# Kernel optimization log

Measured on AMD Instinct MI355X. Metric: run time of the kernel, lower is better.

## Reference

```python
import jax, jax.numpy as jnp
import numpy as np

N_NODES = 50000
N_REL = 8
IN_DIM = 128
HID = 128
N_EDGES = 800000
N_TRIP = 100000


def setup_inputs() -> dict:
    key = jax.random.key(0)
    ks = jax.random.split(key, 12)
    s = 0.05
    return {
        "emb": jax.random.normal(ks[0], (N_NODES, IN_DIM), jnp.float32),
        "W0": jax.random.normal(ks[1], (N_REL, IN_DIM, HID), jnp.float32) * s,
        "root0": jax.random.normal(ks[2], (IN_DIM, HID), jnp.float32) * s,
        "b0": jnp.zeros((HID,), jnp.float32),
        "W1": jax.random.normal(ks[3], (N_REL, HID, HID), jnp.float32) * s,
        "root1": jax.random.normal(ks[4], (HID, HID), jnp.float32) * s,
        "b1": jnp.zeros((HID,), jnp.float32),
        "rel_emb": jax.random.normal(ks[5], (N_REL, HID), jnp.float32),
        "edge_index": jax.random.randint(ks[6], (2, N_EDGES), 0, N_NODES, jnp.int64 if jax.config.read('jax_enable_x64') else jnp.int32),
        "edge_type": jax.random.randint(ks[7], (N_EDGES,), 0, N_REL, jnp.int32),
        "head_idx": jax.random.randint(ks[8], (N_TRIP,), 0, N_NODES, jnp.int32),
        "rel_idx": jax.random.randint(ks[9], (N_TRIP,), 0, N_REL, jnp.int32),
        "tail_idx": jax.random.randint(ks[10], (N_TRIP,), 0, N_NODES, jnp.int32),
    }


def _rgcn_layer(h, W, root, bias, src, dst, edge_type):
    # PyG RGCNConv: per-relation MEAN aggregation of neighbor features at dst,
    # transformed by the relation weight, plus root transform and bias.
    # Mean commutes with the linear map, so aggregate raw features first.
    n, r = N_NODES, N_REL
    seg = dst * r + edge_type  # (E,) joint (dst, relation) segment id
    msg = h[src]               # (E, d) irregular gather
    sums = jax.ops.segment_sum(msg, seg, num_segments=n * r)          # (N*R, d)
    cnt = jax.ops.segment_sum(jnp.ones((src.shape[0],), h.dtype), seg,
                              num_segments=n * r)                     # (N*R,)
    mean = (sums / jnp.maximum(cnt, 1.0)[:, None]).reshape(n, r, -1)  # (N, R, d)
    return jnp.einsum('nrd,rdh->nh', mean, W) + h @ root + bias


def reference(emb, W0, root0, b0, W1, root1, b1, rel_emb,
              edge_index, edge_type, head_idx, rel_idx, tail_idx):
    src = edge_index[0]
    dst = edge_index[1]
    et = edge_type.astype(jnp.int32)
    h = emb
    h = jax.nn.relu(_rgcn_layer(h, W0, root0, b0, src, dst, et))
    h = jax.nn.relu(_rgcn_layer(h, W1, root1, b1, src, dst, et))
    # DistMult score: sum(h_head * r * h_tail)
    score = jnp.sum(h[head_idx] * rel_emb[rel_idx] * h[tail_idx], axis=-1)
    return score
```

## Files before the change

### kernel.cpp

```cpp
#include <hip/hip_runtime.h>
#include <hip/hip_bf16.h>

#define N_NODES 50000
#define N_REL   8
#define DIM     128
#define N_EDGES 800000
#define N_TRIP  100000
#define NSEG    (N_NODES * N_REL)
#define NBUCKET 196
#define CAP     6144

typedef __attribute__((ext_vector_type(8))) short bf16x8;
typedef __attribute__((ext_vector_type(4))) float f32x4;

static __device__ __forceinline__ unsigned short f2b(float f) {
    __hip_bfloat16 h = __float2bfloat16(f);
    return *reinterpret_cast<unsigned short*>(&h);
}
static __device__ __forceinline__ float blo(unsigned int u) {
    return __uint_as_float(u << 16);
}
static __device__ __forceinline__ float bhi(unsigned int u) {
    return __uint_as_float(u & 0xffff0000u);
}
static __device__ __forceinline__ int lds_off(int row, int chunk) {
    return (row * 16 + (chunk ^ (row & 7))) * 8;
}

__global__ __launch_bounds__(256) void bucket_scatter(
        const int* __restrict__ edge_index,
        const int* __restrict__ edge_type,
        int* __restrict__ gcnt,
        unsigned int* __restrict__ slack) {
    __shared__ int hist[NBUCKET];
    __shared__ int cur[NBUCKET];
    int tid = threadIdx.x;
    for (int i = tid; i < NBUCKET; i += 256) hist[i] = 0;
    __syncthreads();
    int base = blockIdx.x * 4096;
    unsigned int w[16];
    int bk[16];
    #pragma unroll
    for (int i = 0; i < 16; ++i) {
        int e = base + i * 256 + tid;
        if (e < N_EDGES) {
            int src = edge_index[e];
            int dst = edge_index[N_EDGES + e];
            int r = edge_type[e];
            w[i] = (unsigned int)src | ((unsigned int)r << 16) |
                   ((unsigned int)(dst & 255) << 19);
            bk[i] = dst >> 8;
            atomicAdd(&hist[bk[i]], 1);
        } else {
            bk[i] = -1;
        }
    }
    __syncthreads();
    for (int i = tid; i < NBUCKET; i += 256)
        cur[i] = atomicAdd(&gcnt[i], hist[i]);
    __syncthreads();
    #pragma unroll
    for (int i = 0; i < 16; ++i) {
        if (bk[i] >= 0) {
            int p = atomicAdd(&cur[bk[i]], 1);
            if (p < CAP) slack[(size_t)bk[i] * CAP + p] = w[i];
        }
    }
}

__global__ void bucket_scan(const int* __restrict__ gcnt,
                            int* __restrict__ gbase,
                            int* __restrict__ offsets) {
    __shared__ int sh[256];
    int t = threadIdx.x;
    int v = (t < NBUCKET) ? gcnt[t] : 0;
    sh[t] = v;
    __syncthreads();
    #pragma unroll
    for (int off = 1; off < 256; off <<= 1) {
        int x = (t >= off) ? sh[t - off] : 0;
        __syncthreads();
        sh[t] += x;
        __syncthreads();
    }
    if (t < NBUCKET) gbase[t] = sh[t] - v;
    if (t == 0) offsets[NSEG] = N_EDGES;
}

__global__ __launch_bounds__(256) void bucket_sort(
        const unsigned int* __restrict__ slack,
        const int* __restrict__ gcnt,
        const int* __restrict__ gbase,
        unsigned int* __restrict__ sorted_pack,
        int* __restrict__ offsets,
        float* __restrict__ invcnt) {
    __shared__ unsigned int ebuf[CAP];
    __shared__ unsigned int obuf[CAP];
    __shared__ int hist[2048];
    __shared__ int excl[2048];
    __shared__ int sh[256];
    int b = blockIdx.x, t = threadIdx.x;
    int n = gcnt[b]; if (n > CAP) n = CAP;
    int bb = gbase[b];
    for (int i = t; i < n; i += 256) ebuf[i] = slack[(size_t)b * CAP + i];
    for (int i = t; i < 2048; i += 256) hist[i] = 0;
    __syncthreads();
    for (int i = t; i < n; i += 256) {
        unsigned int w = ebuf[i];
        int seg = (int)((w >> 19) << 3) | (int)((w >> 16) & 7u);
        atomicAdd(&hist[seg], 1);
    }
    __syncthreads();
    int c[8];
    int s = 0;
    #pragma unroll
    for (int j = 0; j < 8; ++j) { c[j] = hist[t * 8 + j]; s += c[j]; }
    sh[t] = s;
    __syncthreads();
    #pragma unroll
    for (int off = 1; off < 256; off <<= 1) {
        int x = (t >= off) ? sh[t - off] : 0;
        __syncthreads();
        sh[t] += x;
        __syncthreads();
    }
    int ex = sh[t] - s;
    #pragma unroll
    for (int j = 0; j < 8; ++j) { excl[t * 8 + j] = ex; ex += c[j]; }
    __syncthreads();
    #pragma unroll
    for (int j = 0; j < 8; ++j) hist[t * 8 + j] = excl[t * 8 + j];
    __syncthreads();
    for (int i = t; i < n; i += 256) {
        unsigned int w = ebuf[i];
        int seg = (int)((w >> 19) << 3) | (int)((w >> 16) & 7u);
        int p = atomicAdd(&hist[seg], 1);
        obuf[p] = w & 0x7ffffu;
    }
    __syncthreads();
    for (int i = t; i < n; i += 256) sorted_pack[bb + i] = obuf[i];
    int segbase = b * 2048;
    #pragma unroll
    for (int j = 0; j < 8; ++j) {
        int gseg = segbase + t * 8 + j;
        if (gseg < NSEG) {
            offsets[gseg] = bb + excl[t * 8 + j];
            invcnt[gseg] = (c[j] > 0) ? 1.0f / (float)c[j] : 0.f;
        }
    }
}

__global__ void cvt_emb_kernel(const float* __restrict__ src,
                               unsigned short* __restrict__ dst) {
    int i = blockIdx.x * blockDim.x + threadIdx.x;
    const int npair = N_NODES * DIM / 2;
    if (i >= npair) return;
    float2 v = ((const float2*)src)[i];
    unsigned int p = (unsigned int)f2b(v.x) | ((unsigned int)f2b(v.y) << 16);
    ((unsigned int*)dst)[i] = p;
}

__global__ void cvt_w2_kernel(const float* __restrict__ root0,
                              const float* __restrict__ W0,
                              const float* __restrict__ root1,
                              const float* __restrict__ W1,
                              unsigned short* __restrict__ Wt2a,
                              unsigned short* __restrict__ Wt2b) {
    int s = blockIdx.x;
    int n = blockIdx.y;
    int k = threadIdx.x;
    const float* root = blockIdx.z ? root1 : root0;
    const float* W    = blockIdx.z ? W1 : W0;
    unsigned short* Wt2 = blockIdx.z ? Wt2b : Wt2a;
    float v = (s == 0) ? root[k * 128 + n]
                       : W[((size_t)(s - 1) * 128 + k) * 128 + n];
    Wt2[((size_t)s * 128 + n) * 128 + k] = f2b(v);
}

__global__ __launch_bounds__(256) void gemm9_bn32(
        const unsigned short* __restrict__ hb,
        const unsigned short* __restrict__ Wt2,
        unsigned short* __restrict__ Y) {
    __shared__ unsigned short Bs[32 * 16 * 8];

    int tid = threadIdx.x;
    int wave = tid >> 6, lane = tid & 63;
    int wm = wave & 1, wn = wave >> 1;
    int quad = lane >> 4, l16 = lane & 15;
    int row0 = blockIdx.x * 64;
    int col0 = blockIdx.y * 32;

    bf16x8 afr[2][4];
    #pragma unroll
    for (int i = 0; i < 2; ++i) {
        int grow = row0 + wm * 32 + i * 16 + l16;
        if (grow >= N_NODES) grow = N_NODES - 1;
        #pragma unroll
        for (int kk = 0; kk < 4; ++kk)
            afr[i][kk] = *(const bf16x8*)(hb + (size_t)grow * DIM + kk * 32 + quad * 8);
    }

    for (int s = 0; s < 9; ++s) {
        __syncthreads();
        {
            int n = tid >> 3, c0 = (tid & 7) * 2;
            const unsigned short* gp = Wt2 + ((size_t)s * 128 + col0 + n) * 128 + c0 * 8;
            #pragma unroll
            for (int q = 0; q < 2; ++q)
                *(bf16x8*)&Bs[lds_off(n, c0 + q)] = *(const bf16x8*)(gp + q * 8);
        }
        __syncthreads();

        f32x4 acc[2];
        #pragma unroll
        for (int i = 0; i < 2; ++i) acc[i] = (f32x4){0.f, 0.f, 0.f, 0.f};

        #pragma unroll
        for (int kk = 0; kk < 4; ++kk) {
            int chunk = kk * 4 + quad;
            bf16x8 bfr = *(const bf16x8*)&Bs[lds_off(wn * 16 + l16, chunk)];
            #pragma unroll
            for (int i = 0; i < 2; ++i)
                acc[i] = __builtin_amdgcn_mfma_f32_16x16x32_bf16(
                    afr[i][kk], bfr, acc[i], 0, 0, 0);
        }

        unsigned short* Ys = Y + (size_t)s * N_NODES * 128;
        #pragma unroll
        for (int i = 0; i < 2; ++i) {
            int gr0 = row0 + wm * 32 + i * 16 + quad * 4;
            int gc = col0 + wn * 16 + l16;
            #pragma unroll
            for (int r = 0; r < 4; ++r) {
                int grow = gr0 + r;
                if (grow < N_NODES)
                    Ys[(size_t)grow * 128 + gc] = f2b(acc[i][r]);
            }
        }
    }
}

__global__ __launch_bounds__(256) void aggregate_out(
        const unsigned short* __restrict__ Y,
        const float* __restrict__ bias,
        const int* __restrict__ offsets,
        const unsigned int* __restrict__ sorted_pack,
        const float* __restrict__ invcnt,
        unsigned short* __restrict__ hout) {
    int dst = blockIdx.x * 4 + (threadIdx.x >> 6);
    if (dst >= N_NODES) return;
    int lane = threadIdx.x & 63;
    const unsigned int* Yu = (const unsigned int*)Y;

    unsigned int r0 = Yu[(size_t)dst * 64 + lane];
    float a0 = blo(r0), a1 = bhi(r0);

    int beg = offsets[dst * N_REL];
    int end = offsets[dst * N_REL + N_REL];
    for (int base = beg; base < end; base += 64) {
        int np = end - base; if (np > 64) np = 64;
        unsigned int pk = 0; float ivl = 0.f;
        if (lane < np) {
            pk = sorted_pack[base + lane];
            ivl = invcnt[dst * N_REL + (int)(pk >> 16)];
        }
        int j = 0;
        for (; j + 7 < np; j += 8) {
            unsigned int pp[8]; float ii[8];
            #pragma unroll
            for (int q = 0; q < 8; ++q) {
                pp[q] = __shfl((int)pk, j + q, 64);
                ii[q] = __shfl(ivl, j + q, 64);
            }
            unsigned int vv[8];
            #pragma unroll
            for (int q = 0; q < 8; ++q)
                vv[q] = Yu[((size_t)(1 + (pp[q] >> 16)) * N_NODES + (pp[q] & 0xffffu)) * 64 + lane];
            #pragma unroll
            for (int q = 0; q < 8; ++q) {
                a0 = fmaf(blo(vv[q]), ii[q], a0);
                a1 = fmaf(bhi(vv[q]), ii[q], a1);
            }
        }
        for (; j < np; ++j) {
            unsigned int pj = __shfl((int)pk, j, 64);
            float ij = __shfl(ivl, j, 64);
            unsigned int v = Yu[((size_t)(1 + (pj >> 16)) * N_NODES + (pj & 0xffffu)) * 64 + lane];
            a0 = fmaf(blo(v), ij, a0); a1 = fmaf(bhi(v), ij, a1);
        }
    }
    float2 bv = ((const float2*)bias)[lane];
    a0 = fmaxf(a0 + bv.x, 0.f);
    a1 = fmaxf(a1 + bv.y, 0.f);
    unsigned int po = (unsigned int)f2b(a0) | ((unsigned int)f2b(a1) << 16);
    ((unsigned int*)(hout + (size_t)dst * DIM))[lane] = po;
}

__global__ void score_kernel(const unsigned short* __restrict__ hb,
                             const float* __restrict__ rel_emb,
                             const int* __restrict__ head,
                             const int* __restrict__ rel,
                             const int* __restrict__ tail,
                             float* __restrict__ out) {
    int t = blockIdx.x * 4 + (threadIdx.x >> 6);
    if (t >= N_TRIP) return;
    int lane = threadIdx.x & 63;
    unsigned int ph = ((const unsigned int*)(hb + (size_t)head[t] * DIM))[lane];
    unsigned int pt = ((const unsigned int*)(hb + (size_t)tail[t] * DIM))[lane];
    float2 rr = ((const float2*)(rel_emb + (size_t)rel[t] * DIM))[lane];
    float s = blo(ph) * rr.x * blo(pt) + bhi(ph) * rr.y * bhi(pt);
    #pragma unroll
    for (int off = 32; off; off >>= 1) s += __shfl_xor(s, off, 64);
    if (lane == 0) out[t] = s;
}

extern "C" void kernel_launch(void* const* d_in, const int* in_sizes, int n_in,
                              void* d_out, int out_size, void* d_ws, size_t ws_size,
                              hipStream_t stream) {
    const float* emb     = (const float*)d_in[0];
    const float* W0      = (const float*)d_in[1];
    const float* root0   = (const float*)d_in[2];
    const float* b0      = (const float*)d_in[3];
    const float* W1      = (const float*)d_in[4];
    const float* root1   = (const float*)d_in[5];
    const float* b1      = (const float*)d_in[6];
    const float* rel_emb = (const float*)d_in[7];
    const int* edge_index = (const int*)d_in[8];
    const int* edge_type  = (const int*)d_in[9];
    const int* head_idx   = (const int*)d_in[10];
    const int* rel_idx    = (const int*)d_in[11];
    const int* tail_idx   = (const int*)d_in[12];
    float* out = (float*)d_out;

    char* p = (char*)d_ws;
    size_t y_bytes   = (size_t)9 * N_NODES * DIM * sizeof(unsigned short);
    size_t hb_bytes  = (size_t)N_NODES * DIM * sizeof(unsigned short);
    size_t wt2_bytes = (size_t)9 * 128 * 128 * sizeof(unsigned short);
    unsigned short* Y    = (unsigned short*)p; p += y_bytes;
    unsigned short* embb = (unsigned short*)p; p += hb_bytes;
    unsigned short* h1b  = (unsigned short*)p; p += hb_bytes;
    unsigned short* h2b  = (unsigned short*)p; p += hb_bytes;
    unsigned short* Wt2a = (unsigned short*)p; p += wt2_bytes;
    unsigned short* Wt2b = (unsigned short*)p; p += wt2_bytes;
    int* offsets = (int*)p;           p += (size_t)(NSEG + 1) * sizeof(int);
    float* invcnt = (float*)p;        p += (size_t)NSEG * sizeof(float);
    unsigned int* sorted_pack = (unsigned int*)p; p += (size_t)N_EDGES * sizeof(unsigned int);
    unsigned int* slack = (unsigned int*)p; p += (size_t)NBUCKET * CAP * sizeof(unsigned int);
    int* gcnt  = (int*)p;             p += (size_t)NBUCKET * sizeof(int);
    int* gbase = (int*)p;
    (void)ws_size; (void)in_sizes; (void)n_in; (void)out_size;

    dim3 blk256(256);

    hipMemsetAsync(gcnt, 0, (size_t)NBUCKET * sizeof(int), stream);
    bucket_scatter<<<(N_EDGES + 4095) / 4096, blk256, 0, stream>>>(edge_index, edge_type,
                                                                   gcnt, slack);
    bucket_scan<<<1, 256, 0, stream>>>(gcnt, gbase, offsets);
    bucket_sort<<<NBUCKET, blk256, 0, stream>>>(slack, gcnt, gbase, sorted_pack,
                                                offsets, invcnt);

    cvt_emb_kernel<<<(N_NODES * DIM / 2 + 255) / 256, blk256, 0, stream>>>(emb, embb);
    cvt_w2_kernel<<<dim3(9, 128, 2), 128, 0, stream>>>(root0, W0, root1, W1, Wt2a, Wt2b);

    dim3 ggrid((N_NODES + 63) / 64, 4);
    int agrid = (N_NODES + 3) / 4;

    gemm9_bn32<<<ggrid, blk256, 0, stream>>>(embb, Wt2a, Y);
    aggregate_out<<<agrid, blk256, 0, stream>>>(Y, b0, offsets, sorted_pack, invcnt, h1b);

    gemm9_bn32<<<ggrid, blk256, 0, stream>>>(h1b, Wt2b, Y);
    aggregate_out<<<agrid, blk256, 0, stream>>>(Y, b1, offsets, sorted_pack, invcnt, h2b);

    score_kernel<<<(N_TRIP + 3) / 4, blk256, 0, stream>>>(h2b, rel_emb, head_idx, rel_idx,
                                                          tail_idx, out);
}
```

Before: 314.3 us.

## Fuse per-relation mean aggregation with MFMA transform, dropping the 9-slice intermediate

```diff
diff --git a/kernel.cpp b/kernel.cpp
--- a/kernel.cpp
+++ b/kernel.cpp
@@ -6,9 +6,10 @@
 #define DIM     128
 #define N_EDGES 800000
 #define N_TRIP  100000
-#define NSEG    (N_NODES * N_REL)
-#define NBUCKET 196
-#define CAP     6144
+#define NDBLK   196
+#define NB2     (N_REL * NDBLK)
+#define CAP2    1024
+#define NOFF    (N_REL * N_NODES + 1)
 
 typedef __attribute__((ext_vector_type(8))) short bf16x8;
 typedef __attribute__((ext_vector_type(4))) float f32x4;
@@ -32,10 +33,10 @@
         const int* __restrict__ edge_type,
         int* __restrict__ gcnt,
         unsigned int* __restrict__ slack) {
-    __shared__ int hist[NBUCKET];
-    __shared__ int cur[NBUCKET];
+    __shared__ int hist[NB2];
+    __shared__ int cur[NB2];
     int tid = threadIdx.x;
-    for (int i = tid; i < NBUCKET; i += 256) hist[i] = 0;
+    for (int i = tid; i < NB2; i += 256) hist[i] = 0;
     __syncthreads();
     int base = blockIdx.x * 4096;
     unsigned int w[16];
@@ -47,34 +48,40 @@
             int src = edge_index[e];
             int dst = edge_index[N_EDGES + e];
             int r = edge_type[e];
-            w[i] = (unsigned int)src | ((unsigned int)r << 16) |
-                   ((unsigned int)(dst & 255) << 19);
-            bk[i] = dst >> 8;
+            w[i] = (unsigned int)src | ((unsigned int)(dst & 255) << 16);
+            bk[i] = r * NDBLK + (dst >> 8);
             atomicAdd(&hist[bk[i]], 1);
         } else {
             bk[i] = -1;
         }
     }
     __syncthreads();
-    for (int i = tid; i < NBUCKET; i += 256)
+    for (int i = tid; i < NB2; i += 256)
         cur[i] = atomicAdd(&gcnt[i], hist[i]);
     __syncthreads();
     #pragma unroll
     for (int i = 0; i < 16; ++i) {
         if (bk[i] >= 0) {
             int p = atomicAdd(&cur[bk[i]], 1);
-            if (p < CAP) slack[(size_t)bk[i] * CAP + p] = w[i];
+            if (p < CAP2) slack[(size_t)bk[i] * CAP2 + p] = w[i];
         }
     }
 }
 
 __global__ void bucket_scan(const int* __restrict__ gcnt,
                             int* __restrict__ gbase,
-                            int* __restrict__ offsets) {
+                            int* __restrict__ offR) {
     __shared__ int sh[256];
     int t = threadIdx.x;
-    int v = (t < NBUCKET) ? gcnt[t] : 0;
-    sh[t] = v;
+    int c[8];
+    int s = 0;
+    #pragma unroll
+    for (int j = 0; j < 8; ++j) {
+        int idx = t * 8 + j;
+        int v = (idx < NB2) ? gcnt[idx] : 0;
+        c[j] = v; s += v;
+    }
+    sh[t] = s;
     __syncthreads();
     #pragma unroll
     for (int off = 1; off < 256; off <<= 1) {
@@ -83,71 +90,60 @@
         sh[t] += x;
         __syncthreads();
     }
-    if (t < NBUCKET) gbase[t] = sh[t] - v;
-    if (t == 0) offsets[NSEG] = N_EDGES;
+    int ex = sh[t] - s;
+    #pragma unroll
+    for (int j = 0; j < 8; ++j) {
+        int idx = t * 8 + j;
+        if (idx < NB2) gbase[idx] = ex;
+        ex += c[j];
+    }
+    if (t == 0) offR[N_REL * N_NODES] = N_EDGES;
 }
 
 __global__ __launch_bounds__(256) void bucket_sort(
         const unsigned int* __restrict__ slack,
         const int* __restrict__ gcnt,
         const int* __restrict__ gbase,
-        unsigned int* __restrict__ sorted_pack,
-        int* __restrict__ offsets,
-        float* __restrict__ invcnt) {
-    __shared__ unsigned int ebuf[CAP];
-    __shared__ unsigned int obuf[CAP];
-    __shared__ int hist[2048];
-    __shared__ int excl[2048];
+        unsigned int* __restrict__ spack,
+        int* __restrict__ offR) {
+    __shared__ unsigned int ebuf[CAP2];
+    __shared__ unsigned int obuf[CAP2];
+    __shared__ int hist[256];
+    __shared__ int excl[256];
     __shared__ int sh[256];
     int b = blockIdx.x, t = threadIdx.x;
-    int n = gcnt[b]; if (n > CAP) n = CAP;
+    int r = b / NDBLK, dblk = b % NDBLK;
+    int n = gcnt[b]; if (n > CAP2) n = CAP2;
     int bb = gbase[b];
-    for (int i = t; i < n; i += 256) ebuf[i] = slack[(size_t)b * CAP + i];
-    for (int i = t; i < 2048; i += 256) hist[i] = 0;
+    for (int i = t; i < n; i += 256) ebuf[i] = slack[(size_t)b * CAP2 + i];
+    hist[t] = 0;
+    __syncthreads();
+    for (int i = t; i < n; i += 256)
+        atomicAdd(&hist[(ebuf[i] >> 16) & 255], 1);
+    __syncthreads();
+    int c = hist[t];
+    sh[t] = c;
+    __syncthreads();
+    #pragma unroll
+    for (int off = 1; off < 256; off <<= 1) {
+        int x = (t >= off) ? sh[t - off] : 0;
+        __syncthreads();
+        sh[t] += x;
+        __syncthreads();
+    }
+    int ex = sh[t] - c;
+    excl[t] = ex;
+    hist[t] = ex;
     __syncthreads();
     for (int i = t; i < n; i += 256) {
         unsigned int w = ebuf[i];
-        int seg = (int)((w >> 19) << 3) | (int)((w >> 16) & 7u);
-        atomicAdd(&hist[seg], 1);
-    }
-    __syncthreads();
-    int c[8];
-    int s = 0;
-    #pragma unroll
-    for (int j = 0; j < 8; ++j) { c[j] = hist[t * 8 + j]; s += c[j]; }
-    sh[t] = s;
-    __syncthreads();
-    #pragma unroll
-    for (int off = 1; off < 256; off <<= 1) {
-        int x = (t >= off) ? sh[t - off] : 0;
-        __syncthreads();
-        sh[t] += x;
-        __syncthreads();
-    }
-    int ex = sh[t] - s;
-    #pragma unroll
-    for (int j = 0; j < 8; ++j) { excl[t * 8 + j] = ex; ex += c[j]; }
-    __syncthreads();
-    #pragma unroll
-    for (int j = 0; j < 8; ++j) hist[t * 8 + j] = excl[t * 8 + j];
-    __syncthreads();
-    for (int i = t; i < n; i += 256) {
-        unsigned int w = ebuf[i];
-        int seg = (int)((w >> 19) << 3) | (int)((w >> 16) & 7u);
-        int p = atomicAdd(&hist[seg], 1);
-        obuf[p] = w & 0x7ffffu;
-    }
-    __syncthreads();
-    for (int i = t; i < n; i += 256) sorted_pack[bb + i] = obuf[i];
-    int segbase = b * 2048;
-    #pragma unroll
-    for (int j = 0; j < 8; ++j) {
-        int gseg = segbase + t * 8 + j;
-        if (gseg < NSEG) {
-            offsets[gseg] = bb + excl[t * 8 + j];
-            invcnt[gseg] = (c[j] > 0) ? 1.0f / (float)c[j] : 0.f;
-        }
-    }
+        int p = atomicAdd(&hist[(w >> 16) & 255], 1);
+        obuf[p] = w;
+    }
+    __syncthreads();
+    for (int i = t; i < n; i += 256) spack[bb + i] = obuf[i];
+    int dst = dblk * 256 + t;
+    if (dst < N_NODES) offR[r * N_NODES + dst] = bb + excl[t];
 }
 
 __global__ void cvt_emb_kernel(const float* __restrict__ src,
@@ -177,123 +173,144 @@
     Wt2[((size_t)s * 128 + n) * 128 + k] = f2b(v);
 }
 
-__global__ __launch_bounds__(256) void gemm9_bn32(
+__global__ __launch_bounds__(256) void rgcn_fused(
         const unsigned short* __restrict__ hb,
         const unsigned short* __restrict__ Wt2,
-        unsigned short* __restrict__ Y) {
-    __shared__ unsigned short Bs[32 * 16 * 8];
+        const float* __restrict__ bias,
+        const int* __restrict__ offR,
+        const unsigned int* __restrict__ spack,
+        unsigned short* __restrict__ hout) {
+    __shared__ unsigned short Mbuf[64 * 16 * 8];
+    unsigned int* Mb32 = (unsigned int*)Mbuf;
+    const unsigned int* hb32 = (const unsigned int*)hb;
 
     int tid = threadIdx.x;
-    int wave = tid >> 6, lane = tid & 63;
-    int wm = wave & 1, wn = wave >> 1;
+    int wid = tid >> 6, lane = tid & 63;
     int quad = lane >> 4, l16 = lane & 15;
-    int row0 = blockIdx.x * 64;
-    int col0 = blockIdx.y * 32;
-
-    bf16x8 afr[2][4];
-    #pragma unroll
-    for (int i = 0; i < 2; ++i) {
-        int grow = row0 + wm * 32 + i * 16 + l16;
-        if (grow >= N_NODES) grow = N_NODES - 1;
+    int t0 = blockIdx.x * 64;
+    int col0w = wid * 32;
+
+    f32x4 acc[4][2];
+    #pragma unroll
+    for (int mi = 0; mi < 4; ++mi)
+        #pragma unroll
+        for (int ni = 0; ni < 2; ++ni)
+            acc[mi][ni] = (f32x4){0.f, 0.f, 0.f, 0.f};
+
+    {
+        const unsigned short* Wp = Wt2 + ((size_t)(col0w + l16)) * DIM + quad * 8;
+        bf16x8 bf[2][4];
+        #pragma unroll
+        for (int ni = 0; ni < 2; ++ni)
+            #pragma unroll
+            for (int kk = 0; kk < 4; ++kk)
+                bf[ni][kk] = *(const bf16x8*)(Wp + (ni * 16) * DIM + kk * 32);
         #pragma unroll
         for (int kk = 0; kk < 4; ++kk)
-            afr[i][kk] = *(const bf16x8*)(hb + (size_t)grow * DIM + kk * 32 + quad * 8);
-    }
-
-    for (int s = 0; s < 9; ++s) {
-        __syncthreads();
-        {
-            int n = tid >> 3, c0 = (tid & 7) * 2;
-            const unsigned short* gp = Wt2 + ((size_t)s * 128 + col0 + n) * 128 + c0 * 8;
-            #pragma unroll
-            for (int q = 0; q < 2; ++q)
-                *(bf16x8*)&Bs[lds_off(n, c0 + q)] = *(const bf16x8*)(gp + q * 8);
-        }
-        __syncthreads();
-
-        f32x4 acc[2];
-        #pragma unroll
-        for (int i = 0; i < 2; ++i) acc[i] = (f32x4){0.f, 0.f, 0.f, 0.f};
-
-        #pragma unroll
-        for (int kk = 0; kk < 4; ++kk) {
-            int chunk = kk * 4 + quad;
-            bf16x8 bfr = *(const bf16x8*)&Bs[lds_off(wn * 16 + l16, chunk)];
-            #pragma unroll
-            for (int i = 0; i < 2; ++i)
-                acc[i] = __builtin_amdgcn_mfma_f32_16x16x32_bf16(
-                    afr[i][kk], bfr, acc[i], 0, 0, 0);
-        }
-
-        unsigned short* Ys = Y + (size_t)s * N_NODES * 128;
-        #pragma unroll
-        for (int i = 0; i < 2; ++i) {
-            int gr0 = row0 + wm * 32 + i * 16 + quad * 4;
-            int gc = col0 + wn * 16 + l16;
-            #pragma unroll
-            for (int r = 0; r < 4; ++r) {
-                int grow = gr0 + r;
+            #pragma unroll
+            for (int mi = 0; mi < 4; ++mi) {
+                int grow = t0 + mi * 16 + l16;
+                if (grow >= N_NODES) grow = N_NODES - 1;
+                bf16x8 af = *(const bf16x8*)(hb + (size_t)grow * DIM + kk * 32 + quad * 8);
+                #pragma unroll
+                for (int ni = 0; ni < 2; ++ni)
+                    acc[mi][ni] = __builtin_amdgcn_mfma_f32_16x16x32_bf16(
+                        af, bf[ni][kk], acc[mi][ni], 0, 0, 0);
+            }
+    }
+
+    for (int r = 0; r < N_REL; ++r) {
+        const unsigned short* Wp = Wt2 + ((size_t)(1 + r) * DIM + col0w + l16) * DIM + quad * 8;
+        bf16x8 bf[2][4];
+        #pragma unroll
+        for (int ni = 0; ni < 2; ++ni)
+            #pragma unroll
+            for (int kk = 0; kk < 4; ++kk)
+                bf[ni][kk] = *(const bf16x8*)(Wp + (ni * 16) * DIM + kk * 32);
+
+        int d0 = t0 + wid * 16;
+        int ia = d0 < N_NODES ? d0 : N_NODES;
+        int ib = (d0 + 16) < N_NODES ? (d0 + 16) : N_NODES;
+        int beg = offR[r * N_NODES + ia];
+        int end = offR[r * N_NODES + ib];
+        unsigned int flushed = 0;
+        float a0 = 0.f, a1 = 0.f;
+        int curd = -1, cnt = 0;
+        for (int base = beg; base < end; base += 64) {
+            int m = end - base; if (m > 64) m = 64;
+            unsigned int pk = 0;
+            if (lane < m) pk = spack[base + lane];
+            for (int j = 0; j < m; j += 8) {
+                int bc = m - j; if (bc > 8) bc = 8;
+                unsigned int pp[8], vv[8];
+                #pragma unroll
+                for (int q = 0; q < 8; ++q)
+                    if (q < bc) pp[q] = (unsigned int)__shfl((int)pk, j + q, 64);
+                #pragma unroll
+                for (int q = 0; q < 8; ++q)
+                    if (q < bc) vv[q] = hb32[(size_t)(pp[q] & 0xffffu) * 64 + lane];
+                #pragma unroll
+                for (int q = 0; q < 8; ++q) {
+                    if (q < bc) {
+                        int dl = (int)((pp[q] >> 16) & 63u);
+                        float x0 = blo(vv[q]), x1 = bhi(vv[q]);
+                        if (dl != curd) {
+                            if (curd >= 0) {
+                                float inv = __builtin_amdgcn_rcpf((float)cnt);
+                                Mb32[(curd * 16 + ((lane >> 2) ^ (curd & 7))) * 4 + (lane & 3)] =
+                                    (unsigned int)f2b(a0 * inv) |
+                                    ((unsigned int)f2b(a1 * inv) << 16);
+                                flushed |= 1u << (curd & 15);
+                            }
+                            curd = dl; a0 = x0; a1 = x1; cnt = 1;
+                        } else {
+                            a0 += x0; a1 += x1; ++cnt;
+                        }
+                    }
+                }
+            }
+        }
+        if (curd >= 0) {
+            float inv = __builtin_amdgcn_rcpf((float)cnt);
+            Mb32[(curd * 16 + ((lane >> 2) ^ (curd & 7))) * 4 + (lane & 3)] =
+                (unsigned int)f2b(a0 * inv) | ((unsigned int)f2b(a1 * inv) << 16);
+            flushed |= 1u << (curd & 15);
+        }
+        #pragma unroll
+        for (int i = 0; i < 16; ++i) {
+            if (!((flushed >> i) & 1u)) {
+                int row = wid * 16 + i;
+                Mb32[(row * 16 + ((lane >> 2) ^ (row & 7))) * 4 + (lane & 3)] = 0u;
+            }
+        }
+        __syncthreads();
+
+        #pragma unroll
+        for (int kk = 0; kk < 4; ++kk)
+            #pragma unroll
+            for (int mi = 0; mi < 4; ++mi) {
+                bf16x8 af = *(const bf16x8*)&Mbuf[lds_off(mi * 16 + l16, kk * 4 + quad)];
+                #pragma unroll
+                for (int ni = 0; ni < 2; ++ni)
+                    acc[mi][ni] = __builtin_amdgcn_mfma_f32_16x16x32_bf16(
+                        af, bf[ni][kk], acc[mi][ni], 0, 0, 0);
+            }
+        __syncthreads();
+    }
+
+    #pragma unroll
+    for (int ni = 0; ni < 2; ++ni) {
+        int gc = col0w + ni * 16 + l16;
+        float bv = bias[gc];
+        #pragma unroll
+        for (int mi = 0; mi < 4; ++mi)
+            #pragma unroll
+            for (int rr = 0; rr < 4; ++rr) {
+                int grow = t0 + mi * 16 + quad * 4 + rr;
                 if (grow < N_NODES)
-                    Ys[(size_t)grow * 128 + gc] = f2b(acc[i][r]);
-            }
-        }
-    }
-}
-
-__global__ __launch_bounds__(256) void aggregate_out(
-        const unsigned short* __restrict__ Y,
-        const float* __restrict__ bias,
-        const int* __restrict__ offsets,
-        const unsigned int* __restrict__ sorted_pack,
-        const float* __restrict__ invcnt,
-        unsigned short* __restrict__ hout) {
-    int dst = blockIdx.x * 4 + (threadIdx.x >> 6);
-    if (dst >= N_NODES) return;
-    int lane = threadIdx.x & 63;
-    const unsigned int* Yu = (const unsigned int*)Y;
-
-    unsigned int r0 = Yu[(size_t)dst * 64 + lane];
-    float a0 = blo(r0), a1 = bhi(r0);
-
-    int beg = offsets[dst * N_REL];
-    int end = offsets[dst * N_REL + N_REL];
-    for (int base = beg; base < end; base += 64) {
-        int np = end - base; if (np > 64) np = 64;
-        unsigned int pk = 0; float ivl = 0.f;
-        if (lane < np) {
-            pk = sorted_pack[base + lane];
-            ivl = invcnt[dst * N_REL + (int)(pk >> 16)];
-        }
-        int j = 0;
-        for (; j + 7 < np; j += 8) {
-            unsigned int pp[8]; float ii[8];
-            #pragma unroll
-            for (int q = 0; q < 8; ++q) {
-                pp[q] = __shfl((int)pk, j + q, 64);
-                ii[q] = __shfl(ivl, j + q, 64);
-            }
-            unsigned int vv[8];
-            #pragma unroll
-            for (int q = 0; q < 8; ++q)
-                vv[q] = Yu[((size_t)(1 + (pp[q] >> 16)) * N_NODES + (pp[q] & 0xffffu)) * 64 + lane];
-            #pragma unroll
-            for (int q = 0; q < 8; ++q) {
-                a0 = fmaf(blo(vv[q]), ii[q], a0);
-                a1 = fmaf(bhi(vv[q]), ii[q], a1);
-            }
-        }
-        for (; j < np; ++j) {
-            unsigned int pj = __shfl((int)pk, j, 64);
-            float ij = __shfl(ivl, j, 64);
-            unsigned int v = Yu[((size_t)(1 + (pj >> 16)) * N_NODES + (pj & 0xffffu)) * 64 + lane];
-            a0 = fmaf(blo(v), ij, a0); a1 = fmaf(bhi(v), ij, a1);
-        }
-    }
-    float2 bv = ((const float2*)bias)[lane];
-    a0 = fmaxf(a0 + bv.x, 0.f);
-    a1 = fmaxf(a1 + bv.y, 0.f);
-    unsigned int po = (unsigned int)f2b(a0) | ((unsigned int)f2b(a1) << 16);
-    ((unsigned int*)(hout + (size_t)dst * DIM))[lane] = po;
+                    hout[(size_t)grow * DIM + gc] = f2b(fmaxf(acc[mi][ni][rr] + bv, 0.f));
+            }
+    }
 }
 
 __global__ void score_kernel(const unsigned short* __restrict__ hb,
@@ -333,43 +350,35 @@
     float* out = (float*)d_out;
 
     char* p = (char*)d_ws;
-    size_t y_bytes   = (size_t)9 * N_NODES * DIM * sizeof(unsigned short);
     size_t hb_bytes  = (size_t)N_NODES * DIM * sizeof(unsigned short);
     size_t wt2_bytes = (size_t)9 * 128 * 128 * sizeof(unsigned short);
-    unsigned short* Y    = (unsigned short*)p; p += y_bytes;
     unsigned short* embb = (unsigned short*)p; p += hb_bytes;
     unsigned short* h1b  = (unsigned short*)p; p += hb_bytes;
     unsigned short* h2b  = (unsigned short*)p; p += hb_bytes;
     unsigned short* Wt2a = (unsigned short*)p; p += wt2_bytes;
     unsigned short* Wt2b = (unsigned short*)p; p += wt2_bytes;
-    int* offsets = (int*)p;           p += (size_t)(NSEG + 1) * sizeof(int);
-    float* invcnt = (float*)p;        p += (size_t)NSEG * sizeof(float);
-    unsigned int* sorted_pack = (unsigned int*)p; p += (size_t)N_EDGES * sizeof(unsigned int);
-    unsigned int* slack = (unsigned int*)p; p += (size_t)NBUCKET * CAP * sizeof(unsigned int);
-    int* gcnt  = (int*)p;             p += (size_t)NBUCKET * sizeof(int);
-    int* gbase = (int*)p;
+    unsigned int* spack = (unsigned int*)p;   p += (size_t)N_EDGES * sizeof(unsigned int);
+    unsigned int* slack = (unsigned int*)p;   p += (size_t)NB2 * CAP2 * sizeof(unsigned int);
+    int* gcnt  = (int*)p;  p += (size_t)NB2 * sizeof(int);
+    int* gbase = (int*)p;  p += (size_t)NB2 * sizeof(int);
+    int* offR  = (int*)p;  p += (size_t)NOFF * sizeof(int);
     (void)ws_size; (void)in_sizes; (void)n_in; (void)out_size;
 
     dim3 blk256(256);
 
-    hipMemsetAsync(gcnt, 0, (size_t)NBUCKET * sizeof(int), stream);
+    hipMemsetAsync(gcnt, 0, (size_t)NB2 * sizeof(int), stream);
     bucket_scatter<<<(N_EDGES + 4095) / 4096, blk256, 0, stream>>>(edge_index, edge_type,
                                                                    gcnt, slack);
-    bucket_scan<<<1, 256, 0, stream>>>(gcnt, gbase, offsets);
-    bucket_sort<<<NBUCKET, blk256, 0, stream>>>(slack, gcnt, gbase, sorted_pack,
-                                                offsets, invcnt);
+    bucket_scan<<<1, 256, 0, stream>>>(gcnt, gbase, offR);
+    bucket_sort<<<NB2, blk256, 0, stream>>>(slack, gcnt, gbase, spack, offR);
 
     cvt_emb_kernel<<<(N_NODES * DIM / 2 + 255) / 256, blk256, 0, stream>>>(emb, embb);
     cvt_w2_kernel<<<dim3(9, 128, 2), 128, 0, stream>>>(root0, W0, root1, W1, Wt2a, Wt2b);
 
-    dim3 ggrid((N_NODES + 63) / 64, 4);
-    int agrid = (N_NODES + 3) / 4;
-
-    gemm9_bn32<<<ggrid, blk256, 0, stream>>>(embb, Wt2a, Y);
-    aggregate_out<<<agrid, blk256, 0, stream>>>(Y, b0, offsets, sorted_pack, invcnt, h1b);
-
-    gemm9_bn32<<<ggrid, blk256, 0, stream>>>(h1b, Wt2b, Y);
-    aggregate_out<<<agrid, blk256, 0, stream>>>(Y, b1, offsets, sorted_pack, invcnt, h2b);
+    int fgrid = (N_NODES + 63) / 64;
+
+    rgcn_fused<<<fgrid, blk256, 0, stream>>>(embb, Wt2a, b0, offR, spack, h1b);
+    rgcn_fused<<<fgrid, blk256, 0, stream>>>(h1b, Wt2b, b1, offR, spack, h2b);
 
     score_kernel<<<(N_TRIP + 3) / 4, blk256, 0, stream>>>(h2b, rel_emb, head_idx, rel_idx,
                                                           tail_idx, out);
```

New measurement: 365.3 us. 1.16x slower.

## Fuse per-relation mean aggregation and GEMM into one RGCN layer kernel

Applied to the files above, without the earlier changes.

```diff
diff --git a/kernel.cpp b/kernel.cpp
--- a/kernel.cpp
+++ b/kernel.cpp
@@ -22,9 +22,6 @@
 }
 static __device__ __forceinline__ float bhi(unsigned int u) {
     return __uint_as_float(u & 0xffff0000u);
-}
-static __device__ __forceinline__ int lds_off(int row, int chunk) {
-    return (row * 16 + (chunk ^ (row & 7))) * 8;
 }
 
 __global__ __launch_bounds__(256) void bucket_scatter(
@@ -92,8 +89,7 @@
         const int* __restrict__ gcnt,
         const int* __restrict__ gbase,
         unsigned int* __restrict__ sorted_pack,
-        int* __restrict__ offsets,
-        float* __restrict__ invcnt) {
+        int* __restrict__ offsets) {
     __shared__ unsigned int ebuf[CAP];
     __shared__ unsigned int obuf[CAP];
     __shared__ int hist[2048];
@@ -135,7 +131,7 @@
         unsigned int w = ebuf[i];
         int seg = (int)((w >> 19) << 3) | (int)((w >> 16) & 7u);
         int p = atomicAdd(&hist[seg], 1);
-        obuf[p] = w & 0x7ffffu;
+        obuf[p] = w;
     }
     __syncthreads();
     for (int i = t; i < n; i += 256) sorted_pack[bb + i] = obuf[i];
@@ -143,10 +139,7 @@
     #pragma unroll
     for (int j = 0; j < 8; ++j) {
         int gseg = segbase + t * 8 + j;
-        if (gseg < NSEG) {
-            offsets[gseg] = bb + excl[t * 8 + j];
-            invcnt[gseg] = (c[j] > 0) ? 1.0f / (float)c[j] : 0.f;
-        }
+        if (gseg < NSEG) offsets[gseg] = bb + excl[t * 8 + j];
     }
 }
 
@@ -177,123 +170,143 @@
     Wt2[((size_t)s * 128 + n) * 128 + k] = f2b(v);
 }
 
-__global__ __launch_bounds__(256) void gemm9_bn32(
+#define FLUSH()                                                                \
+    do {                                                                       \
+        float inv_ = __builtin_amdgcn_rcpf((float)cnt);                        \
+        int row_ = curk >> 3;                                                  \
+        int c_ = (curk & 7) * 16 + (lane >> 2);                                \
+        int swz_ = (c_ & ~7) | ((c_ ^ row_) & 7);                              \
+        MtU[row_ * 512 + swz_ * 4 + (lane & 3)] =                              \
+            (unsigned int)f2b(a0 * inv_) | ((unsigned int)f2b(a1 * inv_) << 16);\
+        flushed |= 1u << (curk & 31);                                          \
+    } while (0)
+
+#define CONSUME(w_, v_)                                                        \
+    do {                                                                       \
+        int k_ = (int)((((w_) >> 19) & 15u) * 8u + (((w_) >> 16) & 7u));       \
+        float x0_ = blo(v_), x1_ = bhi(v_);                                    \
+        if (k_ != curk) {                                                      \
+            if (curk >= 0) FLUSH();                                            \
+            curk = k_; a0 = x0_; a1 = x1_; cnt = 1;                            \
+        } else { a0 += x0_; a1 += x1_; ++cnt; }                                \
+    } while (0)
+
+__global__ __launch_bounds__(256) void rgcn_fused(
         const unsigned short* __restrict__ hb,
         const unsigned short* __restrict__ Wt2,
-        unsigned short* __restrict__ Y) {
-    __shared__ unsigned short Bs[32 * 16 * 8];
-
-    int tid = threadIdx.x;
-    int wave = tid >> 6, lane = tid & 63;
-    int wm = wave & 1, wn = wave >> 1;
-    int quad = lane >> 4, l16 = lane & 15;
-    int row0 = blockIdx.x * 64;
-    int col0 = blockIdx.y * 32;
-
-    bf16x8 afr[2][4];
-    #pragma unroll
-    for (int i = 0; i < 2; ++i) {
-        int grow = row0 + wm * 32 + i * 16 + l16;
-        if (grow >= N_NODES) grow = N_NODES - 1;
-        #pragma unroll
-        for (int kk = 0; kk < 4; ++kk)
-            afr[i][kk] = *(const bf16x8*)(hb + (size_t)grow * DIM + kk * 32 + quad * 8);
-    }
-
-    for (int s = 0; s < 9; ++s) {
-        __syncthreads();
-        {
-            int n = tid >> 3, c0 = (tid & 7) * 2;
-            const unsigned short* gp = Wt2 + ((size_t)s * 128 + col0 + n) * 128 + c0 * 8;
-            #pragma unroll
-            for (int q = 0; q < 2; ++q)
-                *(bf16x8*)&Bs[lds_off(n, c0 + q)] = *(const bf16x8*)(gp + q * 8);
-        }
-        __syncthreads();
-
-        f32x4 acc[2];
-        #pragma unroll
-        for (int i = 0; i < 2; ++i) acc[i] = (f32x4){0.f, 0.f, 0.f, 0.f};
-
-        #pragma unroll
-        for (int kk = 0; kk < 4; ++kk) {
-            int chunk = kk * 4 + quad;
-            bf16x8 bfr = *(const bf16x8*)&Bs[lds_off(wn * 16 + l16, chunk)];
-            #pragma unroll
-            for (int i = 0; i < 2; ++i)
-                acc[i] = __builtin_amdgcn_mfma_f32_16x16x32_bf16(
-                    afr[i][kk], bfr, acc[i], 0, 0, 0);
-        }
-
-        unsigned short* Ys = Y + (size_t)s * N_NODES * 128;
-        #pragma unroll
-        for (int i = 0; i < 2; ++i) {
-            int gr0 = row0 + wm * 32 + i * 16 + quad * 4;
-            int gc = col0 + wn * 16 + l16;
-            #pragma unroll
-            for (int r = 0; r < 4; ++r) {
-                int grow = gr0 + r;
-                if (grow < N_NODES)
-                    Ys[(size_t)grow * 128 + gc] = f2b(acc[i][r]);
-            }
-        }
-    }
-}
-
-__global__ __launch_bounds__(256) void aggregate_out(
-        const unsigned short* __restrict__ Y,
         const float* __restrict__ bias,
         const int* __restrict__ offsets,
-        const unsigned int* __restrict__ sorted_pack,
-        const float* __restrict__ invcnt,
+        const unsigned int* __restrict__ spack,
         unsigned short* __restrict__ hout) {
-    int dst = blockIdx.x * 4 + (threadIdx.x >> 6);
-    if (dst >= N_NODES) return;
-    int lane = threadIdx.x & 63;
-    const unsigned int* Yu = (const unsigned int*)Y;
-
-    unsigned int r0 = Yu[(size_t)dst * 64 + lane];
-    float a0 = blo(r0), a1 = bhi(r0);
-
-    int beg = offsets[dst * N_REL];
-    int end = offsets[dst * N_REL + N_REL];
-    for (int base = beg; base < end; base += 64) {
-        int np = end - base; if (np > 64) np = 64;
-        unsigned int pk = 0; float ivl = 0.f;
-        if (lane < np) {
-            pk = sorted_pack[base + lane];
-            ivl = invcnt[dst * N_REL + (int)(pk >> 16)];
+    __shared__ unsigned short Mt[16 * 1024];
+    unsigned int* MtU = (unsigned int*)Mt;
+    const unsigned int* hb32 = (const unsigned int*)hb;
+
+    int tid = threadIdx.x;
+    int wid = tid >> 6, lane = tid & 63;
+    int quad = lane >> 4, l16 = lane & 15;
+    int t0 = blockIdx.x * 16;
+
+    int beg = offsets[(t0 + wid * 4) * 8];
+    int end = offsets[(t0 + wid * 4 + 4) * 8];
+
+    int m = end - beg; if (m > 64) m = 64;
+    unsigned int pk = 0;
+    if (lane < m) pk = spack[beg + lane];
+
+    f32x4 acc[2];
+    acc[0] = (f32x4){0.f, 0.f, 0.f, 0.f};
+    acc[1] = (f32x4){0.f, 0.f, 0.f, 0.f};
+
+    {
+        const unsigned short* Wp = Wt2 + (size_t)(wid * 32 + l16) * DIM + quad * 8;
+        bf16x8 b0[4], b1[4];
+        #pragma unroll
+        for (int kk = 0; kk < 4; ++kk) {
+            b0[kk] = *(const bf16x8*)(Wp + kk * 32);
+            b1[kk] = *(const bf16x8*)(Wp + 16 * DIM + kk * 32);
+        }
+        #pragma unroll
+        for (int kk = 0; kk < 4; ++kk) {
+            bf16x8 af = *(const bf16x8*)(hb + (size_t)(t0 + l16) * DIM + kk * 32 + quad * 8);
+            acc[0] = __builtin_amdgcn_mfma_f32_16x16x32_bf16(af, b0[kk], acc[0], 0, 0, 0);
+            acc[1] = __builtin_amdgcn_mfma_f32_16x16x32_bf16(af, b1[kk], acc[1], 0, 0, 0);
+        }
+    }
+
+    float a0 = 0.f, a1 = 0.f;
+    int curk = -1, cnt = 0;
+    unsigned int flushed = 0;
+    int base = beg;
+    while (base < end) {
+        int nbase = base + 64;
+        unsigned int pkn = 0;
+        if (nbase < end) {
+            int mn = end - nbase; if (mn > 64) mn = 64;
+            if (lane < mn) pkn = spack[nbase + lane];
         }
         int j = 0;
-        for (; j + 7 < np; j += 8) {
-            unsigned int pp[8]; float ii[8];
-            #pragma unroll
-            for (int q = 0; q < 8; ++q) {
-                pp[q] = __shfl((int)pk, j + q, 64);
-                ii[q] = __shfl(ivl, j + q, 64);
-            }
-            unsigned int vv[8];
+        for (; j + 8 <= m; j += 8) {
+            unsigned int pp[8], vv[8];
             #pragma unroll
             for (int q = 0; q < 8; ++q)
-                vv[q] = Yu[((size_t)(1 + (pp[q] >> 16)) * N_NODES + (pp[q] & 0xffffu)) * 64 + lane];
+                pp[q] = (unsigned int)__shfl((int)pk, j + q, 64);
             #pragma unroll
-            for (int q = 0; q < 8; ++q) {
-                a0 = fmaf(blo(vv[q]), ii[q], a0);
-                a1 = fmaf(bhi(vv[q]), ii[q], a1);
-            }
-        }
-        for (; j < np; ++j) {
-            unsigned int pj = __shfl((int)pk, j, 64);
-            float ij = __shfl(ivl, j, 64);
-            unsigned int v = Yu[((size_t)(1 + (pj >> 16)) * N_NODES + (pj & 0xffffu)) * 64 + lane];
-            a0 = fmaf(blo(v), ij, a0); a1 = fmaf(bhi(v), ij, a1);
-        }
-    }
-    float2 bv = ((const float2*)bias)[lane];
-    a0 = fmaxf(a0 + bv.x, 0.f);
-    a1 = fmaxf(a1 + bv.y, 0.f);
-    unsigned int po = (unsigned int)f2b(a0) | ((unsigned int)f2b(a1) << 16);
-    ((unsigned int*)(hout + (size_t)dst * DIM))[lane] = po;
+            for (int q = 0; q < 8; ++q)
+                vv[q] = hb32[(size_t)(pp[q] & 0xffffu) * 64 + lane];
+            #pragma unroll
+            for (int q = 0; q < 8; ++q) CONSUME(pp[q], vv[q]);
+        }
+        for (; j < m; ++j) {
+            unsigned int p1 = (unsigned int)__shfl((int)pk, j, 64);
+            unsigned int v1 = hb32[(size_t)(p1 & 0xffffu) * 64 + lane];
+            CONSUME(p1, v1);
+        }
+        base = nbase; pk = pkn;
+        m = end - base; if (m > 64) m = 64;
+    }
+    if (curk >= 0) FLUSH();
+    #pragma unroll 1
+    for (int i = 0; i < 32; ++i) {
+        if (!((flushed >> i) & 1u)) {
+            int k = wid * 32 + i;
+            int row = k >> 3;
+            int c = (k & 7) * 16 + (lane >> 2);
+            int swz = (c & ~7) | ((c ^ row) & 7);
+            MtU[row * 512 + swz * 4 + (lane & 3)] = 0u;
+        }
+    }
+    __syncthreads();
+
+    #pragma unroll
+    for (int s = 1; s < 9; ++s) {
+        const unsigned short* Wp = Wt2 + ((size_t)s * 128 + wid * 32 + l16) * DIM + quad * 8;
+        bf16x8 b0[4], b1[4];
+        #pragma unroll
+        for (int kk = 0; kk < 4; ++kk) {
+            b0[kk] = *(const bf16x8*)(Wp + kk * 32);
+            b1[kk] = *(const bf16x8*)(Wp + 16 * DIM + kk * 32);
+        }
+        #pragma unroll
+        for (int kk = 0; kk < 4; ++kk) {
+            int c = (s - 1) * 16 + kk * 4 + quad;
+            int swz = (c & ~7) | ((c ^ l16) & 7);
+            bf16x8 af = *(const bf16x8*)&Mt[l16 * 1024 + swz * 8];
+            acc[0] = __builtin_amdgcn_mfma_f32_16x16x32_bf16(af, b0[kk], acc[0], 0, 0, 0);
+            acc[1] = __builtin_amdgcn_mfma_f32_16x16x32_bf16(af, b1[kk], acc[1], 0, 0, 0);
+        }
+    }
+
+    #pragma unroll
+    for (int ni = 0; ni < 2; ++ni) {
+        int gc = wid * 32 + ni * 16 + l16;
+        float bv = bias[gc];
+        #pragma unroll
+        for (int rr = 0; rr < 4; ++rr) {
+            int grow = t0 + quad * 4 + rr;
+            hout[(size_t)grow * DIM + gc] = f2b(fmaxf(acc[ni][rr] + bv, 0.f));
+        }
+    }
 }
 
 __global__ void score_kernel(const unsigned short* __restrict__ hb,
@@ -333,21 +346,18 @@
     float* out = (float*)d_out;
 
     char* p = (char*)d_ws;
-    size_t y_bytes   = (size_t)9 * N_NODES * DIM * sizeof(unsigned short);
     size_t hb_bytes  = (size_t)N_NODES * DIM * sizeof(unsigned short);
     size_t wt2_bytes = (size_t)9 * 128 * 128 * sizeof(unsigned short);
-    unsigned short* Y    = (unsigned short*)p; p += y_bytes;
     unsigned short* embb = (unsigned short*)p; p += hb_bytes;
     unsigned short* h1b  = (unsigned short*)p; p += hb_bytes;
     unsigned short* h2b  = (unsigned short*)p; p += hb_bytes;
     unsigned short* Wt2a = (unsigned short*)p; p += wt2_bytes;
     unsigned short* Wt2b = (unsigned short*)p; p += wt2_bytes;
-    int* offsets = (int*)p;           p += (size_t)(NSEG + 1) * sizeof(int);
-    float* invcnt = (float*)p;        p += (size_t)NSEG * sizeof(float);
-    unsigned int* sorted_pack = (unsigned int*)p; p += (size_t)N_EDGES * sizeof(unsigned int);
-    unsigned int* slack = (unsigned int*)p; p += (size_t)NBUCKET * CAP * sizeof(unsigned int);
-    int* gcnt  = (int*)p;             p += (size_t)NBUCKET * sizeof(int);
-    int* gbase = (int*)p;
+    unsigned int* spack = (unsigned int*)p;   p += (size_t)N_EDGES * sizeof(unsigned int);
+    unsigned int* slack = (unsigned int*)p;   p += (size_t)NBUCKET * CAP * sizeof(unsigned int);
+    int* gcnt  = (int*)p;  p += (size_t)NBUCKET * sizeof(int);
+    int* gbase = (int*)p;  p += (size_t)NBUCKET * sizeof(int);
+    int* offsets = (int*)p;
     (void)ws_size; (void)in_sizes; (void)n_in; (void)out_size;
 
     dim3 blk256(256);
@@ -356,20 +366,15 @@
     bucket_scatter<<<(N_EDGES + 4095) / 4096, blk256, 0, stream>>>(edge_index, edge_type,
                                                                    gcnt, slack);
     bucket_scan<<<1, 256, 0, stream>>>(gcnt, gbase, offsets);
-    bucket_sort<<<NBUCKET, blk256, 0, stream>>>(slack, gcnt, gbase, sorted_pack,
-                                                offsets, invcnt);
+    bucket_sort<<<NBUCKET, blk256, 0, stream>>>(slack, gcnt, gbase, spack, offsets);
 
     cvt_emb_kernel<<<(N_NODES * DIM / 2 + 255) / 256, blk256, 0, stream>>>(emb, embb);
     cvt_w2_kernel<<<dim3(9, 128, 2), 128, 0, stream>>>(root0, W0, root1, W1, Wt2a, Wt2b);
 
-    dim3 ggrid((N_NODES + 63) / 64, 4);
-    int agrid = (N_NODES + 3) / 4;
-
-    gemm9_bn32<<<ggrid, blk256, 0, stream>>>(embb, Wt2a, Y);
-    aggregate_out<<<agrid, blk256, 0, stream>>>(Y, b0, offsets, sorted_pack, invcnt, h1b);
-
-    gemm9_bn32<<<ggrid, blk256, 0, stream>>>(h1b, Wt2b, Y);
-    aggregate_out<<<agrid, blk256, 0, stream>>>(Y, b1, offsets, sorted_pack, invcnt, h2b);
+    int fgrid = N_NODES / 16;
+
+    rgcn_fused<<<fgrid, blk256, 0, stream>>>(embb, Wt2a, b0, offsets, spack, h1b);
+    rgcn_fused<<<fgrid, blk256, 0, stream>>>(h1b, Wt2b, b1, offsets, spack, h2b);
 
     score_kernel<<<(N_TRIP + 3) / 4, blk256, 0, stream>>>(h2b, rel_emb, head_idx, rel_idx,
                                                           tail_idx, out);
```

Result: slower. 420.4 us (+33.8%).
